# Performance work log

Measured on AMD Instinct MI355X. Metric: run time of the kernel, lower is better.

The kernel has to match this reference:

```python
import jax, jax.numpy as jnp
import numpy as np

N_GENE, N_CPG, N_MIRNA = 20000, 60000, 2000
HID, H, NL = 128, 8, 2
C = HID // H
B = 64
NEG_SLOPE = 0.2
LN_EPS = 1e-5
# edge types in HeteroConv order: (src_node_idx, dst_node_idx); node order: 0=gene,1=cpg,2=mirna
EDGE_META = [(1, 0), (0, 1), (2, 0), (0, 2), (0, 0), (0, 0), (1, 1), (2, 2)]


def layernorm(x, g, b):
    mu = jnp.mean(x, axis=-1, keepdims=True)
    var = jnp.mean(jnp.square(x - mu), axis=-1, keepdims=True)
    return (x - mu) * jax.lax.rsqrt(var + LN_EPS) * g + b


def gatv2_conv(x_src, x_dst, ei, Wl, Wr, att, bias):
    """PyG GATv2Conv, add_self_loops=False, concat heads, eval mode (no dropout)."""
    src, dst = ei[0], ei[1]
    n_dst = x_dst.shape[0]
    hs = (x_src @ Wl).reshape(-1, H, C)   # lin_l -> source features [Ns,H,C]
    hd = (x_dst @ Wr).reshape(-1, H, C)   # lin_r -> target features [Nd,H,C]
    e = jax.nn.leaky_relu(hs[src] + hd[dst], NEG_SLOPE)   # [E,H,C]
    logits = jnp.einsum('ehc,hc->eh', e, att)             # [E,H]
    # segment softmax over destination nodes
    m = jax.ops.segment_max(logits, dst, num_segments=n_dst)
    a = jnp.exp(logits - m[dst])
    s = jax.ops.segment_sum(a, dst, num_segments=n_dst)
    alpha = a / (s[dst] + 1e-16)                          # [E,H]
    msg = (hs[src] * alpha[:, :, None]).reshape(-1, HID)  # [E,HID]
    out = jax.ops.segment_sum(msg, dst, num_segments=n_dst)
    return out + bias


def setup_inputs() -> dict:
    key = jax.random.key(0)
    ks = list(jax.random.split(key, 40))
    nk = lambda: ks.pop()
    rn = lambda shape, s=0.05: jax.random.normal(nk(), shape, jnp.float32) * s

    def edges(E, Ns, Nd):
        src = jax.random.randint(nk(), (E,), 0, Ns, jnp.int32)
        dst = jax.random.randint(nk(), (E,), 0, Nd, jnp.int32)
        return jnp.stack([src, dst])

    def self_loops(N):
        ar = jnp.arange(N, dtype=jnp.int32)
        return jnp.stack([ar, ar])

    inp = {
        'batch_gene': rn((B, N_GENE), 1.0),
        'batch_meth': rn((B, N_CPG), 1.0),
        'batch_mirna': rn((B, N_MIRNA), 1.0),
        'emb_gene': rn((N_GENE, HID)),
        'emb_cpg': rn((N_CPG, HID)),
        'emb_mirna': rn((N_MIRNA, HID)),
        'Wl': rn((NL, 8, HID, HID)),
        'Wr': rn((NL, 8, HID, HID)),
        'att': rn((NL, 8, H, C)),
        'bias': rn((NL, 8, HID), 0.01),
        'ln_gamma': jnp.ones((NL, 3, HID), jnp.float32),
        'ln_beta': jnp.zeros((NL, 3, HID), jnp.float32),
        'out_gamma': jnp.ones((3, HID), jnp.float32),
        'out_beta': jnp.zeros((3, HID), jnp.float32),
        'ei_cg': edges(500000, N_CPG, N_GENE),
        'ei_gc': edges(500000, N_GENE, N_CPG),
        'ei_mg': edges(150000, N_MIRNA, N_GENE),
        'ei_gm': edges(150000, N_GENE, N_MIRNA),
        'ei_gg': edges(500000, N_GENE, N_GENE),
        'ei_sg': self_loops(N_GENE),
        'ei_sc': self_loops(N_CPG),
        'ei_sm': self_loops(N_MIRNA),
    }
    return inp


def forward(batch_gene, batch_meth, batch_mirna, emb_gene, emb_cpg, emb_mirna,
            Wl, Wr, att, bias, ln_gamma, ln_beta, out_gamma, out_beta, edge_list):
    x = [emb_gene, emb_cpg, emb_mirna]  # 0=gene,1=cpg,2=mirna
    for l in range(NL):
        agg = [jnp.zeros_like(x[0]), jnp.zeros_like(x[1]), jnp.zeros_like(x[2])]
        for t, (ei, (si, di)) in enumerate(zip(edge_list, EDGE_META)):
            agg[di] = agg[di] + gatv2_conv(x[si], x[di], ei,
                                           Wl[l, t], Wr[l, t], att[l, t], bias[l, t])
        # ELU + residual + LayerNorm per node type (dropout=0 / eval)
        x = [layernorm(x[i] + jax.nn.elu(agg[i]), ln_gamma[l, i], ln_beta[l, i])
             for i in range(3)]
    z_gene = layernorm(batch_gene @ x[0] / np.sqrt(N_GENE), out_gamma[0], out_beta[0])
    z_cpg = layernorm(batch_meth @ x[1] / np.sqrt(N_CPG), out_gamma[1], out_beta[1])
    z_mirna = layernorm(batch_mirna @ x[2] / np.sqrt(N_MIRNA), out_gamma[2], out_beta[2])
    return (z_gene, z_cpg, z_mirna)


def reference(batch_gene, batch_meth, batch_mirna, emb_gene, emb_cpg, emb_mirna,
              Wl, Wr, att, bias, ln_gamma, ln_beta, out_gamma, out_beta,
              ei_cg, ei_gc, ei_mg, ei_gm, ei_gg, ei_sg, ei_sc, ei_sm):
    edge_list = [ei_cg, ei_gc, ei_mg, ei_gm, ei_gg, ei_sg, ei_sc, ei_sm]
    return forward(batch_gene, batch_meth, batch_mirna, emb_gene, emb_cpg, emb_mirna,
                   Wl, Wr, att, bias, ln_gamma, ln_beta, out_gamma, out_beta, edge_list)
```

## Files before the change

kernel.cpp:

```cpp
#include <hip/hip_runtime.h>
#include <math.h>

typedef __attribute__((ext_vector_type(4))) float f32x4;
typedef __attribute__((ext_vector_type(2))) float f32x2;
typedef __attribute__((ext_vector_type(8))) short bf16x8;

__device__ __forceinline__ float b2f(unsigned short u) {
  return __uint_as_float(((unsigned)u) << 16);
}
__device__ __forceinline__ unsigned short f2b(float f) {
  unsigned x = __float_as_uint(f);
  unsigned r = (x + 0x7FFFu + ((x >> 16) & 1u)) >> 16;
  return (unsigned short)r;
}
__device__ __forceinline__ f32x2 bf2x2(unsigned u) {
  f32x2 r;
  r.x = __uint_as_float(u << 16);
  r.y = __uint_as_float(u & 0xFFFF0000u);
  return r;
}
__device__ __forceinline__ f32x2 pk_max(f32x2 a, f32x2 b) {
#if __has_builtin(__builtin_elementwise_max)
  return __builtin_elementwise_max(a, b);
#else
  f32x2 r; r.x = fmaxf(a.x, b.x); r.y = fmaxf(a.y, b.y); return r;
#endif
}
__device__ __forceinline__ f32x2 pk_fma(f32x2 a, f32x2 b, f32x2 c) {
#if __has_builtin(__builtin_elementwise_fma)
  return __builtin_elementwise_fma(a, b, c);
#else
  f32x2 r; r.x = fmaf(a.x, b.x, c.x); r.y = fmaf(a.y, b.y, c.y); return r;
#endif
}

#if __has_builtin(__builtin_amdgcn_cvt_pk_f32_fp8)
template<bool HI>
__device__ __forceinline__ f32x2 fp8x2_dec(unsigned w) {
  return __builtin_amdgcn_cvt_pk_f32_fp8(w, HI);
}
#else
__device__ __forceinline__ float fp8_dec1(unsigned b) {
  unsigned s = b >> 7, e = (b >> 3) & 15, m = b & 7;
  float v = (e == 0) ? (float)m * 0.001953125f
                     : __uint_as_float(((e - 7 + 127) << 23) | (m << 20));
  return s ? -v : v;
}
template<bool HI>
__device__ __forceinline__ f32x2 fp8x2_dec(unsigned w) {
  unsigned h = HI ? (w >> 16) : w;
  f32x2 r; r.x = fp8_dec1(h & 0xFF); r.y = fp8_dec1((h >> 8) & 0xFF);
  return r;
}
#endif
#if __has_builtin(__builtin_amdgcn_cvt_pk_fp8_f32)
__device__ __forceinline__ unsigned char fp8_enc_byte(float a) {
  return (unsigned char)(__builtin_amdgcn_cvt_pk_fp8_f32(a, a, 0, false) & 0xFF);
}
#else
__device__ __forceinline__ unsigned fp8_enc1(float f) {
  unsigned s = (__float_as_uint(f) >> 31) << 7;
  float a = fabsf(f);
  if (a >= 448.f) return s | 0x7E;
  if (a < 0.015625f) {
    int m = (int)(a * 512.f + 0.5f);
    return s | (unsigned)(m > 7 ? 7 : m);
  }
  int ex; (void)frexpf(a, &ex);
  int E = ex - 1;
  float sig = a * exp2f((float)(-E));
  int m = (int)((sig - 1.f) * 8.f + 0.5f);
  if (m == 8) { m = 0; E += 1; }
  if (E > 8) return s | 0x7E;
  return s | (unsigned)((E + 7) << 3) | (unsigned)m;
}
__device__ __forceinline__ unsigned char fp8_enc_byte(float a) {
  return (unsigned char)fp8_enc1(a);
}
#endif

__global__ __launch_bounds__(256) void prep_w(
    const float* __restrict__ Wl, const float* __restrict__ Wr,
    unsigned short* __restrict__ wt)
{
  int elem = blockIdx.x * 256 + threadIdx.x;
  int mat = elem >> 14;
  int c = (elem >> 7) & 127;
  int k = elem & 127;
  const float* srcb = (mat & 1) ? Wr : Wl;
  wt[elem] = f2b(srcb[((long)(mat >> 1) << 14) + (k << 7) + c]);
}

__global__ __launch_bounds__(256) void cast_all(
    const float* __restrict__ e0, const float* __restrict__ e1,
    const float* __restrict__ e2, unsigned short* __restrict__ x0,
    unsigned short* __restrict__ x1, unsigned short* __restrict__ x2,
    int n0, int n1, int n2)
{
  int i = blockIdx.x * 256 + threadIdx.x;
  const float* s; unsigned short* d; int loc = i;
  if (loc < n0) { s = e0; d = x0; }
  else {
    loc -= n0;
    if (loc < n1) { s = e1; d = x1; }
    else { loc -= n1; if (loc >= n2) return; s = e2; d = x2; }
  }
  float4 v = *(const float4*)(s + (long)loc * 4);
  ushort4 o = {f2b(v.x), f2b(v.y), f2b(v.z), f2b(v.w)};
  *(ushort4*)(d + (long)loc * 4) = o;
}

__global__ __launch_bounds__(128) void prep_bias(
    const float* __restrict__ bias, float* __restrict__ bsum)
{
  int c = threadIdx.x;
  const int TM[3] = {0x35, 0x42, 0x88};
  for (int l = 0; l < 2; ++l)
    for (int ty = 0; ty < 3; ++ty) {
      float s = 0.f;
      for (int t = 0; t < 8; ++t)
        if (TM[ty] & (1 << t)) s += bias[(l * 8 + t) * 128 + c];
      bsum[(l * 3 + ty) * 128 + c] = s;
    }
}

__device__ __forceinline__ void mproj_tile(
    char* lx, char* lw, const unsigned short* __restrict__ xb,
    const unsigned short* __restrict__ wt, void* __restrict__ outv,
    int N, long r0, int tid, int mode)
{
#pragma unroll
  for (int i = 0; i < 8; ++i) {
    int ch = i * 256 + tid;
    int row = ch >> 4, k0 = (ch & 15) << 3;
    uint4 xv = {0u, 0u, 0u, 0u};
    if (r0 + row < N) xv = *(const uint4*)(xb + (r0 + row) * 128 + k0);
    *(uint4*)(lx + ((row * 256 + k0 * 2) ^ ((row & 7) << 4))) = xv;
    uint4 wv = *(const uint4*)(wt + (long)ch * 8);
    *(uint4*)(lw + ((ch * 16) ^ ((row & 7) << 4))) = wv;
  }
  __syncthreads();

  const int lane = tid & 63;
  const int lr = lane & 15, lk = lane >> 4;
  const int rbase = (tid >> 6) * 32;
  f32x4 acc[2][8] = {};
#pragma unroll
  for (int kb = 0; kb < 4; ++kb) {
    int k = kb * 32 + lk * 8;
    int ra = rbase + lr;
    bf16x8 a0 = *(const bf16x8*)(lx + ((ra * 256 + k * 2) ^ ((ra & 7) << 4)));
    int rb = rbase + 16 + lr;
    bf16x8 a1 = *(const bf16x8*)(lx + ((rb * 256 + k * 2) ^ ((rb & 7) << 4)));
#pragma unroll
    for (int cc = 0; cc < 8; ++cc) {
      int col = cc * 16 + lr;
      bf16x8 bfr = *(const bf16x8*)(lw + ((col * 256 + k * 2) ^ ((col & 7) << 4)));
      acc[0][cc] = __builtin_amdgcn_mfma_f32_16x16x32_bf16(a0, bfr, acc[0][cc], 0, 0, 0);
      acc[1][cc] = __builtin_amdgcn_mfma_f32_16x16x32_bf16(a1, bfr, acc[1][cc], 0, 0, 0);
    }
  }
  __syncthreads();
#pragma unroll
  for (int rt = 0; rt < 2; ++rt) {
    int rowb = rbase + rt * 16 + lk * 4;
#pragma unroll
    for (int cc = 0; cc < 8; ++cc) {
      int col = cc * 16 + lr;
#pragma unroll
      for (int q = 0; q < 4; ++q) {
        long row = r0 + rowb + q;
        if (row < N) {
          if (mode == 3)
            ((unsigned char*)outv)[row * 128 + col] = fp8_enc_byte(acc[rt][cc][q]);
          else if (mode == 2)
            ((unsigned short*)outv)[row * 128 + col] = f2b(acc[rt][cc][q]);
          else
            ((float*)outv)[row * 128 + col] = acc[rt][cc][q];
        }
      }
    }
  }
}

struct PJob { const unsigned short* x; const unsigned short* wt; void* out; int N; int mode; };
struct PArgs { PJob j[13]; int off[14]; };

__global__ __launch_bounds__(256) void mproj_all(PArgs a)
{
  __shared__ __align__(16) char lx[32768];
  __shared__ __align__(16) char lw[32768];
  int blk = blockIdx.x, t = 0;
  while (blk >= a.off[t + 1]) ++t;
  const PJob& J = a.j[t];
  mproj_tile(lx, lw, J.x, J.wt, J.out, J.N, (long)(blk - a.off[t]) * 128,
             threadIdx.x, J.mode);
}

struct BArgs {
  const int* src[5]; const int* dst[5];
  int* cnt[5];
  int* tmp[5];
  int* rs[5];
  int* csrc[5];
  int E[5], Nd[5], NB[5], B[5];
  int cOff[6], fOff[6];
};

__global__ __launch_bounds__(256) void bucket_count(BArgs a)
{
  __shared__ int h[512];
  int blk = blockIdx.x, t = 0;
  while (blk >= a.cOff[t + 1]) ++t;
  int lb = blk - a.cOff[t];
  int B = a.B[t], NB = a.NB[t], E = a.E[t];
  for (int i = threadIdx.x; i < B; i += 256) h[i] = 0;
  __syncthreads();
  const int* dst = a.dst[t];
  int base = lb * 4096;
#pragma unroll
  for (int j = 0; j < 16; ++j) {
    int e = base + j * 256 + threadIdx.x;
    if (e < E) atomicAdd(&h[dst[e] >> 7], 1);
  }
  __syncthreads();
  int* cnt = a.cnt[t];
  for (int b = threadIdx.x; b < B; b += 256) cnt[b * NB + lb] = h[b];
}

__global__ __launch_bounds__(1024) void bucket_scan(BArgs a)
{
  int t = blockIdx.x;
  int n = a.B[t] * a.NB[t];
  int* dp = a.cnt[t];
  __shared__ int wsum[16];
  __shared__ int sbase, ctot;
  int tid = threadIdx.x;
  int lane = tid & 63, wid = tid >> 6;
  if (tid == 0) sbase = 0;
  __syncthreads();
  for (int chunk = 0; chunk < n; chunk += 16384) {
    int idx0 = chunk + tid * 16;
    int v[16], lsum = 0;
#pragma unroll
    for (int j = 0; j < 16; ++j) {
      v[j] = (idx0 + j < n) ? dp[idx0 + j] : 0;
      lsum += v[j];
    }
    int sc = lsum;
#pragma unroll
    for (int o = 1; o < 64; o <<= 1) {
      int u = __shfl_up(sc, o);
      if (lane >= o) sc += u;
    }
    if (lane == 63) wsum[wid] = sc;
    __syncthreads();
    if (wid == 0) {
      int w = (lane < 16) ? wsum[lane] : 0;
      int s2 = w;
#pragma unroll
      for (int o = 1; o < 16; o <<= 1) {
        int u = __shfl_up(s2, o);
        if (lane >= o) s2 += u;
      }
      if (lane < 16) wsum[lane] = s2 - w;
      if (lane == 15) ctot = s2;
    }
    __syncthreads();
    int excl = sbase + wsum[wid] + (sc - lsum);
#pragma unroll
    for (int j = 0; j < 16; ++j) {
      if (idx0 + j < n) dp[idx0 + j] = excl;
      excl += v[j];
    }
    __syncthreads();
    if (tid == 0) sbase += ctot;
    __syncthreads();
  }
}

__global__ __launch_bounds__(256) void bucket_scatter(BArgs a)
{
  __shared__ int cur[512];
  int blk = blockIdx.x, t = 0;
  while (blk >= a.cOff[t + 1]) ++t;
  int lb = blk - a.cOff[t];
  int B = a.B[t], NB = a.NB[t], E = a.E[t];
  const int* cnt = a.cnt[t];
  for (int b = threadIdx.x; b < B; b += 256) cur[b] = cnt[b * NB + lb];
  __syncthreads();
  const int* src = a.src[t];
  const int* dst = a.dst[t];
  int* tmp = a.tmp[t];
  int base = lb * 4096;
#pragma unroll
  for (int j = 0; j < 16; ++j) {
    int e = base + j * 256 + threadIdx.x;
    if (e < E) {
      int dv = dst[e];
      int pos = atomicAdd(&cur[dv >> 7], 1);
      tmp[pos] = ((dv & 127) << 16) | src[e];
    }
  }
}

__global__ __launch_bounds__(256) void bucket_finalize(BArgs a)
{
  __shared__ int h[128], sc[128], ex[128], cur[128];
  int blk = blockIdx.x, t = 0;
  while (blk >= a.fOff[t + 1]) ++t;
  int b = blk - a.fOff[t];
  int B = a.B[t], NB = a.NB[t], E = a.E[t], Nd = a.Nd[t];
  const int* cnt = a.cnt[t];
  const int* tmp = a.tmp[t];
  int* rs = a.rs[t];
  int* csrc = a.csrc[t];
  int tid = threadIdx.x;
  int beg = cnt[b * NB];
  int end = (b + 1 < B) ? cnt[(b + 1) * NB] : E;
  if (tid < 128) h[tid] = 0;
  __syncthreads();
  for (int i = beg + tid; i < end; i += 256)
    atomicAdd(&h[tmp[i] >> 16], 1);
  __syncthreads();
  if (tid < 128) sc[tid] = h[tid];
  __syncthreads();
#pragma unroll
  for (int off = 1; off < 128; off <<= 1) {
    int v = (tid < 128 && tid >= off) ? sc[tid - off] : 0;
    __syncthreads();
    if (tid < 128) sc[tid] += v;
    __syncthreads();
  }
  if (tid < 128) {
    ex[tid] = sc[tid] - h[tid];
    cur[tid] = 0;
    int dg = b * 128 + tid;
    if (dg < Nd) rs[dg] = beg + ex[tid];
  }
  if (b == B - 1 && tid == 0) rs[Nd] = E;
  __syncthreads();
  for (int i = beg + tid; i < end; i += 256) {
    int v = tmp[i];
    int d = v >> 16;
    int r = atomicAdd(&cur[d], 1);
    csrc[beg + ex[d] + r] = v & 0xFFFF;
  }
}

struct GSeg {
  const int* rs[3]; const int* csrc[3];
  const unsigned char* hs[3]; const unsigned short* hd[3];
  const float* att[3];
  const float* aggSelf;
  const float* xin;
  float* xf; unsigned short* xb;
  const float* bsum;
  const float* gam; const float* bet;
  int Nd; int ntypes;
};
struct GArgs { GSeg s[3]; int off[4]; };

__global__ __launch_bounds__(256) void gat_gather_ln(GArgs g)
{
  int blk = blockIdx.x, si = 0;
  while (blk >= g.off[si + 1]) ++si;
  const GSeg& sg = g.s[si];
  int d = (blk - g.off[si]) * 4 + (threadIdx.x >> 6);
  if (d >= sg.Nd) return;
  int lane = threadIdx.x & 63;
  int q = lane >> 4, j = lane & 15;
  f32x2 T0 = {0.f, 0.f}, T1 = {0.f, 0.f}, T2 = {0.f, 0.f}, T3 = {0.f, 0.f};
  for (int k = 0; k < sg.ntypes; ++k) {
    const float* ap = sg.att[k] + 8 * j;
    float4 aa = *(const float4*)ap;
    float4 ab = *(const float4*)(ap + 4);
    f32x2 A0 = {aa.x, aa.y}, A1 = {aa.z, aa.w};
    f32x2 A2 = {ab.x, ab.y}, A3 = {ab.z, ab.w};
    uint4 hu = *((const uint4*)(sg.hd[k] + (long)d * 128) + j);
    f32x2 H0 = bf2x2(hu.x), H1 = bf2x2(hu.y);
    f32x2 H2 = bf2x2(hu.z), H3 = bf2x2(hu.w);
    const int* cs = sg.csrc[k];
    const unsigned char* hsk = sg.hs[k];
    int beg = sg.rs[k][d], end = sg.rs[k][d + 1];
    f32x2 n0 = {0.f, 0.f}, n1 = {0.f, 0.f}, n2 = {0.f, 0.f}, n3 = {0.f, 0.f};
    float D = 0.f;

#define GA_EDGE(U)                                                          \
    {                                                                       \
      f32x2 h0 = fp8x2_dec<false>((U).x), h1 = fp8x2_dec<true>((U).x);      \
      f32x2 h2 = fp8x2_dec<false>((U).y), h3 = fp8x2_dec<true>((U).y);      \
      f32x2 v0 = h0 + H0, v1 = h1 + H1, v2 = h2 + H2, v3 = h3 + H3;         \
      v0 = pk_max(v0, v0 * 0.2f);                                           \
      v1 = pk_max(v1, v1 * 0.2f);                                           \
      v2 = pk_max(v2, v2 * 0.2f);                                           \
      v3 = pk_max(v3, v3 * 0.2f);                                           \
      f32x2 pv = pk_fma(v0, A0, pk_fma(v1, A1, pk_fma(v2, A2, v3 * A3)));   \
      float p = pv.x + pv.y;                                                \
      p += __shfl_xor(p, 1);                                                \
      float a = __expf(fminf(p, 60.f));                                     \
      f32x2 av = {a, a};                                                    \
      n0 = pk_fma(h0, av, n0);                                              \
      n1 = pk_fma(h1, av, n1);                                              \
      n2 = pk_fma(h2, av, n2);                                              \
      n3 = pk_fma(h3, av, n3);                                              \
      D += a;                                                               \
    }

    int i = beg + q;
    int sA = (i < end) ? cs[i] : 0;
    int sB = (i + 4 < end) ? cs[i + 4] : 0;
    for (; i + 4 < end; i += 8) {
      uint2 u0 = *((const uint2*)(hsk + (long)sA * 128) + j);
      uint2 u1 = *((const uint2*)(hsk + (long)sB * 128) + j);
      sA = (i + 8 < end) ? cs[i + 8] : 0;
      sB = (i + 12 < end) ? cs[i + 12] : 0;
      GA_EDGE(u0);
      GA_EDGE(u1);
    }
    if (i < end) {
      uint2 u = *((const uint2*)(hsk + (long)sA * 128) + j);
      GA_EDGE(u);
    }
#undef GA_EDGE

#pragma unroll
    for (int o = 16; o < 64; o <<= 1) {
      n0.x += __shfl_xor(n0.x, o); n0.y += __shfl_xor(n0.y, o);
      n1.x += __shfl_xor(n1.x, o); n1.y += __shfl_xor(n1.y, o);
      n2.x += __shfl_xor(n2.x, o); n2.y += __shfl_xor(n2.y, o);
      n3.x += __shfl_xor(n3.x, o); n3.y += __shfl_xor(n3.y, o);
      D += __shfl_xor(D, o);
    }
    float inv = 1.f / (D + 1e-16f);
    f32x2 iv = {inv, inv};
    T0 = pk_fma(n0, iv, T0);
    T1 = pk_fma(n1, iv, T1);
    T2 = pk_fma(n2, iv, T2);
    T3 = pk_fma(n3, iv, T3);
  }

  long base = (long)d * 128 + 8 * j;
  float4 sA0 = *(const float4*)(sg.aggSelf + base);
  float4 sA1 = *(const float4*)(sg.aggSelf + base + 4);
  float4 bb0 = *(const float4*)(sg.bsum + 8 * j);
  float4 bb1 = *(const float4*)(sg.bsum + 8 * j + 4);
  float v[8];
  v[0] = sA0.x + T0.x + bb0.x; v[1] = sA0.y + T0.y + bb0.y;
  v[2] = sA0.z + T1.x + bb0.z; v[3] = sA0.w + T1.y + bb0.w;
  v[4] = sA1.x + T2.x + bb1.x; v[5] = sA1.y + T2.y + bb1.y;
  v[6] = sA1.z + T3.x + bb1.z; v[7] = sA1.w + T3.y + bb1.w;
#pragma unroll
  for (int c = 0; c < 8; ++c) v[c] = v[c] > 0.f ? v[c] : __expf(v[c]) - 1.f;
  float4 xi0 = *(const float4*)(sg.xin + base);
  float4 xi1 = *(const float4*)(sg.xin + base + 4);
  float xr[8] = {xi0.x + v[0], xi0.y + v[1], xi0.z + v[2], xi0.w + v[3],
                 xi1.x + v[4], xi1.y + v[5], xi1.z + v[6], xi1.w + v[7]};
  float ssum = ((xr[0] + xr[1]) + (xr[2] + xr[3])) +
               ((xr[4] + xr[5]) + (xr[6] + xr[7]));
#pragma unroll
  for (int o = 1; o < 16; o <<= 1) ssum += __shfl_xor(ssum, o);
  float mu = ssum * 0.0078125f;
  float qs = 0.f;
#pragma unroll
  for (int c = 0; c < 8; ++c) { float dd = xr[c] - mu; qs += dd * dd; }
#pragma unroll
  for (int o = 1; o < 16; o <<= 1) qs += __shfl_xor(qs, o);
  float rr = rsqrtf(qs * 0.0078125f + 1e-5f);
  float4 g0 = *(const float4*)(sg.gam + 8 * j);
  float4 g1 = *(const float4*)(sg.gam + 8 * j + 4);
  float4 e0 = *(const float4*)(sg.bet + 8 * j);
  float4 e1 = *(const float4*)(sg.bet + 8 * j + 4);
  float y[8];
  y[0] = (xr[0] - mu) * rr * g0.x + e0.x;
  y[1] = (xr[1] - mu) * rr * g0.y + e0.y;
  y[2] = (xr[2] - mu) * rr * g0.z + e0.z;
  y[3] = (xr[3] - mu) * rr * g0.w + e0.w;
  y[4] = (xr[4] - mu) * rr * g1.x + e1.x;
  y[5] = (xr[5] - mu) * rr * g1.y + e1.y;
  y[6] = (xr[6] - mu) * rr * g1.z + e1.z;
  y[7] = (xr[7] - mu) * rr * g1.w + e1.w;
  if (q == 0) {
    float4 o0 = {y[0], y[1], y[2], y[3]};
    float4 o1 = {y[4], y[5], y[6], y[7]};
    *(float4*)(sg.xf + base) = o0;
    *(float4*)(sg.xf + base + 4) = o1;
    uint4 ub;
    ub.x = (unsigned)f2b(y[0]) | ((unsigned)f2b(y[1]) << 16);
    ub.y = (unsigned)f2b(y[2]) | ((unsigned)f2b(y[3]) << 16);
    ub.z = (unsigned)f2b(y[4]) | ((unsigned)f2b(y[5]) << 16);
    ub.w = (unsigned)f2b(y[6]) | ((unsigned)f2b(y[7]) << 16);
    *(uint4*)(sg.xb + base) = ub;
  }
}

struct ZArgs {
  const float* batch[3]; const float* x[3]; float* zp[3]; int N[3];
  int off[4];
};

__global__ __launch_bounds__(256) void zgemm_all(ZArgs z)
{
  __shared__ __align__(16) float xl[64 * 128];
  __shared__ __align__(16) float bl[64 * 65];
  int blk = blockIdx.x, s = 0;
  while (blk >= z.off[s + 1]) ++s;
  int chunk = blk - z.off[s];
  const float* batch = z.batch[s];
  const float* x = z.x[s];
  int N = z.N[s];
  int tid = threadIdx.x;
  int n0 = chunk * 64;
  for (int i = tid; i < 64 * 128; i += 256) {
    int nn = i >> 7;
    xl[i] = (n0 + nn < N) ? x[(long)(n0 + nn) * 128 + (i & 127)] : 0.f;
  }
  for (int i = tid; i < 64 * 64; i += 256) {
    int b = i >> 6, nn = i & 63;
    bl[nn * 65 + b] = (n0 + nn < N) ? batch[(long)b * N + n0 + nn] : 0.f;
  }
  __syncthreads();
  int cg = (tid & 31) * 4;
  int bg = (tid >> 5) * 8;
  float acc[8][4] = {};
  for (int nn = 0; nn < 64; ++nn) {
    float4 xv = *(const float4*)(xl + nn * 128 + cg);
#pragma unroll
    for (int i = 0; i < 8; ++i) {
      float bv = bl[nn * 65 + bg + i];
      acc[i][0] = fmaf(bv, xv.x, acc[i][0]);
      acc[i][1] = fmaf(bv, xv.y, acc[i][1]);
      acc[i][2] = fmaf(bv, xv.z, acc[i][2]);
      acc[i][3] = fmaf(bv, xv.w, acc[i][3]);
    }
  }
  float* zp = z.zp[s] + (long)chunk * 8192;
#pragma unroll
  for (int i = 0; i < 8; ++i) {
    float4 v = {acc[i][0], acc[i][1], acc[i][2], acc[i][3]};
    *(float4*)(zp + (bg + i) * 128 + cg) = v;
  }
}

__global__ __launch_bounds__(256) void zfinal(
    const float* __restrict__ zp0, const float* __restrict__ zp1,
    const float* __restrict__ zp2, int G0, int G1, int G2,
    float s0, float s1, float s2, const float* __restrict__ gam,
    const float* __restrict__ bet, float* __restrict__ out)
{
  int blk = blockIdx.x;
  int ty = blk >> 4;
  int rowL = (blk & 15) * 4 + (threadIdx.x >> 6);
  int lane = threadIdx.x & 63;
  const float* zp = ty == 0 ? zp0 : (ty == 1 ? zp1 : zp2);
  int G = ty == 0 ? G0 : (ty == 1 ? G1 : G2);
  float sc = ty == 0 ? s0 : (ty == 1 ? s1 : s2);
  long i0 = rowL * 128 + lane, i1 = i0 + 64;
  float a0[8], a1[8];
#pragma unroll
  for (int u = 0; u < 8; ++u) { a0[u] = 0.f; a1[u] = 0.f; }
  int g = 0;
  for (; g + 8 <= G; g += 8) {
#pragma unroll
    for (int u = 0; u < 8; ++u) {
      a0[u] += zp[(long)(g + u) * 8192 + i0];
      a1[u] += zp[(long)(g + u) * 8192 + i1];
    }
  }
  for (; g < G; ++g) { a0[0] += zp[(long)g * 8192 + i0]; a1[0] += zp[(long)g * 8192 + i1]; }
  float x0 = (((a0[0] + a0[1]) + (a0[2] + a0[3])) + ((a0[4] + a0[5]) + (a0[6] + a0[7]))) * sc;
  float x1 = (((a1[0] + a1[1]) + (a1[2] + a1[3])) + ((a1[4] + a1[5]) + (a1[6] + a1[7]))) * sc;
  float s = x0 + x1;
#pragma unroll
  for (int o = 32; o > 0; o >>= 1) s += __shfl_xor(s, o);
  float mu = s * 0.0078125f;
  float d0 = x0 - mu, d1 = x1 - mu;
  float qv = d0 * d0 + d1 * d1;
#pragma unroll
  for (int o = 32; o > 0; o >>= 1) qv += __shfl_xor(qv, o);
  float r = rsqrtf(qv * 0.0078125f + 1e-5f);
  long base = (long)(ty * 64 + rowL) * 128;
  out[base + lane]      = d0 * r * gam[ty * 128 + lane]      + bet[ty * 128 + lane];
  out[base + 64 + lane] = d1 * r * gam[ty * 128 + 64 + lane] + bet[ty * 128 + 64 + lane];
}

extern "C" void kernel_launch(void* const* d_in, const int* in_sizes, int n_in,
                              void* d_out, int out_size, void* d_ws, size_t ws_size,
                              hipStream_t stream)
{
  const float* batchp[3] = {(const float*)d_in[0], (const float*)d_in[1],
                            (const float*)d_in[2]};
  const float* emb[3] = {(const float*)d_in[3], (const float*)d_in[4],
                         (const float*)d_in[5]};
  const float* Wl   = (const float*)d_in[6];
  const float* Wr   = (const float*)d_in[7];
  const float* att  = (const float*)d_in[8];
  const float* bias = (const float*)d_in[9];
  const float* lng  = (const float*)d_in[10];
  const float* lnb  = (const float*)d_in[11];
  const float* outg = (const float*)d_in[12];
  const float* outb = (const float*)d_in[13];
  const int* eiP[8]; int E[8];
  for (int t = 0; t < 8; ++t) { eiP[t] = (const int*)d_in[14 + t]; E[t] = in_sizes[14 + t] / 2; }
  int Nn[3] = {in_sizes[3] / 128, in_sizes[4] / 128, in_sizes[5] / 128};
  long Ntot = (long)Nn[0] + Nn[1] + Nn[2];

  const int SI[5] = {1, 0, 2, 0, 0};
  const int DI[5] = {0, 1, 0, 2, 0};

  char* p = (char*)d_ws;
  auto carve = [&](size_t b) -> void* {
    void* r = (void*)p; p += (b + 255) & ~(size_t)255; return r;
  };
  float* xf[3];
  for (int ty = 0; ty < 3; ++ty) xf[ty] = (float*)carve((size_t)Nn[ty] * 128 * 4);
  unsigned short* xb[3];
  for (int ty = 0; ty < 3; ++ty) xb[ty] = (unsigned short*)carve((size_t)Nn[ty] * 128 * 2);
  float* aggAll = (float*)carve((size_t)Ntot * 128 * 4);
  float* agg[3] = {aggAll, aggAll + (long)Nn[0] * 128, aggAll + ((long)Nn[0] + Nn[1]) * 128};
  unsigned short* hdT[5];
  char* projRegion = p;
  for (int t = 0; t < 5; ++t) hdT[t] = (unsigned short*)carve((size_t)Nn[DI[t]] * 128 * 2);
  long hsElems = 0;
  for (int t = 0; t < 5; ++t) hsElems += (long)Nn[SI[t]] * 128;
  unsigned char* hs8base = (unsigned char*)carve((size_t)hsElems);
  unsigned char* hs8T[5];
  {
    unsigned char* q8 = hs8base;
    for (int t = 0; t < 5; ++t) { hs8T[t] = q8; q8 += (long)Nn[SI[t]] * 128; }
  }
  float* bsumBuf = (float*)carve(2 * 3 * 128 * 4);
  unsigned short* wtb = (unsigned short*)carve((size_t)32 * 16384 * 2);

  int nch[3];
  for (int ty = 0; ty < 3; ++ty) nch[ty] = (Nn[ty] + 63) / 64;
  float* zpBase = (float*)carve((size_t)(nch[0] + nch[1] + nch[2]) * 8192 * 4);
  float* zp[3];
  zp[0] = zpBase;
  zp[1] = zp[0] + (long)nch[0] * 8192;
  zp[2] = zp[1] + (long)nch[1] * 8192;
  (void)projRegion;

  BArgs ba;
  {
    int cOff = 0, fOff = 0;
    for (int t = 0; t < 5; ++t) {
      int nd = Nn[DI[t]];
      ba.src[t] = eiP[t];
      ba.dst[t] = eiP[t] + E[t];
      ba.E[t] = E[t];
      ba.Nd[t] = nd;
      ba.NB[t] = (E[t] + 4095) / 4096;
      ba.B[t] = (nd + 127) / 128;
      ba.cnt[t] = (int*)carve((size_t)ba.B[t] * ba.NB[t] * 4);
      ba.tmp[t] = (int*)carve((size_t)E[t] * 4);
      ba.rs[t] = (int*)carve((size_t)(nd + 1) * 4);
      ba.csrc[t] = (int*)carve((size_t)E[t] * 4);
      ba.cOff[t] = cOff; cOff += ba.NB[t];
      ba.fOff[t] = fOff; fOff += ba.B[t];
    }
    ba.cOff[5] = cOff;
    ba.fOff[5] = fOff;
  }
  if ((size_t)(p - (char*)d_ws) > ws_size) return;

  auto WTB = [&](int l, int t, int which) {
    return wtb + ((long)((l * 8 + t) * 2 + which) << 14);
  };

  prep_w<<<2048, 256, 0, stream>>>(Wl, Wr, wtb);
  {
    int n0 = Nn[0] * 32, n1 = Nn[1] * 32, n2 = Nn[2] * 32;
    cast_all<<<(int)((n0 + n1 + n2 + 255) / 256), 256, 0, stream>>>(
        emb[0], emb[1], emb[2], xb[0], xb[1], xb[2], n0, n1, n2);
  }
  prep_bias<<<1, 128, 0, stream>>>(bias, bsumBuf);

  bucket_count<<<ba.cOff[5], 256, 0, stream>>>(ba);
  bucket_scan<<<5, 1024, 0, stream>>>(ba);
  bucket_scatter<<<ba.cOff[5], 256, 0, stream>>>(ba);
  bucket_finalize<<<ba.fOff[5], 256, 0, stream>>>(ba);

  const int GT[3][3] = {{0, 2, 4}, {1, -1, -1}, {3, -1, -1}};
  const int GN[3] = {3, 1, 1};

  for (int l = 0; l < 2; ++l) {
    const float* xinf[3] = {l == 0 ? emb[0] : xf[0],
                            l == 0 ? emb[1] : xf[1],
                            l == 0 ? emb[2] : xf[2]};
    PArgs pa;
    {
      int off = 0, j = 0;
      auto add = [&](const unsigned short* x, const unsigned short* wt,
                     void* out, int N, int mode) {
        pa.j[j] = {x, wt, out, N, mode};
        pa.off[j] = off;
        off += (N + 127) / 128;
        ++j;
      };
      for (int t = 0; t < 5; ++t) add(xb[SI[t]], WTB(l, t, 0), hs8T[t], Nn[SI[t]], 3);
      for (int t = 0; t < 5; ++t) add(xb[DI[t]], WTB(l, t, 1), hdT[t], Nn[DI[t]], 2);
      for (int ty = 0; ty < 3; ++ty) add(xb[ty], WTB(l, 5 + ty, 0), agg[ty], Nn[ty], 0);
      pa.off[13] = off;
      mproj_all<<<off, 256, 0, stream>>>(pa);
    }
    GArgs ga;
    {
      int off = 0;
      for (int s = 0; s < 3; ++s) {
        GSeg& sg = ga.s[s];
        sg.aggSelf = agg[s];
        sg.xin = xinf[s];
        sg.xf = xf[s];
        sg.xb = xb[s];
        sg.bsum = bsumBuf + (long)(l * 3 + s) * 128;
        sg.gam = lng + (long)(l * 3 + s) * 128;
        sg.bet = lnb + (long)(l * 3 + s) * 128;
        sg.Nd = Nn[s];
        sg.ntypes = GN[s];
        for (int k = 0; k < GN[s]; ++k) {
          int t = GT[s][k];
          sg.rs[k] = ba.rs[t];
          sg.csrc[k] = ba.csrc[t];
          sg.hs[k] = hs8T[t];
          sg.hd[k] = hdT[t];
          sg.att[k] = att + (long)(l * 8 + t) * 128;
        }
        ga.off[s] = off;
        off += (Nn[s] + 3) / 4;
      }
      ga.off[3] = off;
      gat_gather_ln<<<off, 256, 0, stream>>>(ga);
    }
  }

  ZArgs za;
  {
    int off = 0;
    for (int ty = 0; ty < 3; ++ty) {
      za.batch[ty] = batchp[ty];
      za.x[ty] = xf[ty];
      za.zp[ty] = zp[ty];
      za.N[ty] = Nn[ty];
      za.off[ty] = off;
      off += nch[ty];
    }
    za.off[3] = off;
    zgemm_all<<<off, 256, 0, stream>>>(za);
  }
  zfinal<<<48, 256, 0, stream>>>(
      zp[0], zp[1], zp[2], nch[0], nch[1], nch[2],
      (float)(1.0 / sqrt((double)Nn[0])), (float)(1.0 / sqrt((double)Nn[1])),
      (float)(1.0 / sqrt((double)Nn[2])), outg, outb, (float*)d_out);
}
```

Measured before the change: 560.3 us.

## Reuse staged input tile across multiple weight projections per block

The projection kernel now loads each 128-row bf16 input tile into shared memory once and loops over up to four weight matrices that share that input, writing each output in its own format. Before, every projection re-read the same input rows from global memory in a separate block. This cuts redundant input reads. In exchange there are fewer, longer blocks (gene rows split into two jobs of 4 and 3 weights), which lowers parallelism and adds extra barriers between weight reloads.

```diff
diff --git a/kernel.cpp b/kernel.cpp
--- a/kernel.cpp
+++ b/kernel.cpp
@@ -124,77 +124,87 @@
     }
 }
 
-__device__ __forceinline__ void mproj_tile(
-    char* lx, char* lw, const unsigned short* __restrict__ xb,
-    const unsigned short* __restrict__ wt, void* __restrict__ outv,
-    int N, long r0, int tid, int mode)
-{
+struct MPJob {
+  const unsigned short* x; int N; int nw;
+  const unsigned short* wt[4]; void* out[4]; int mode[4];
+};
+struct MPArgs { MPJob j[4]; int off[5]; };
+
+__global__ __launch_bounds__(256) void mproj_multi(MPArgs a)
+{
+  __shared__ __align__(16) char lx[32768];
+  __shared__ __align__(16) char lw[32768];
+  int blk = blockIdx.x, t = 0;
+  while (blk >= a.off[t + 1]) ++t;
+  const MPJob& J = a.j[t];
+  const long r0 = (long)(blk - a.off[t]) * 128;
+  const int tid = threadIdx.x;
+  const int N = J.N;
+
 #pragma unroll
   for (int i = 0; i < 8; ++i) {
     int ch = i * 256 + tid;
     int row = ch >> 4, k0 = (ch & 15) << 3;
     uint4 xv = {0u, 0u, 0u, 0u};
-    if (r0 + row < N) xv = *(const uint4*)(xb + (r0 + row) * 128 + k0);
+    if (r0 + row < N) xv = *(const uint4*)(J.x + (r0 + row) * 128 + k0);
     *(uint4*)(lx + ((row * 256 + k0 * 2) ^ ((row & 7) << 4))) = xv;
-    uint4 wv = *(const uint4*)(wt + (long)ch * 8);
-    *(uint4*)(lw + ((ch * 16) ^ ((row & 7) << 4))) = wv;
-  }
-  __syncthreads();
+  }
 
   const int lane = tid & 63;
   const int lr = lane & 15, lk = lane >> 4;
   const int rbase = (tid >> 6) * 32;
-  f32x4 acc[2][8] = {};
-#pragma unroll
-  for (int kb = 0; kb < 4; ++kb) {
-    int k = kb * 32 + lk * 8;
-    int ra = rbase + lr;
-    bf16x8 a0 = *(const bf16x8*)(lx + ((ra * 256 + k * 2) ^ ((ra & 7) << 4)));
-    int rb = rbase + 16 + lr;
-    bf16x8 a1 = *(const bf16x8*)(lx + ((rb * 256 + k * 2) ^ ((rb & 7) << 4)));
-#pragma unroll
-    for (int cc = 0; cc < 8; ++cc) {
-      int col = cc * 16 + lr;
-      bf16x8 bfr = *(const bf16x8*)(lw + ((col * 256 + k * 2) ^ ((col & 7) << 4)));
-      acc[0][cc] = __builtin_amdgcn_mfma_f32_16x16x32_bf16(a0, bfr, acc[0][cc], 0, 0, 0);
-      acc[1][cc] = __builtin_amdgcn_mfma_f32_16x16x32_bf16(a1, bfr, acc[1][cc], 0, 0, 0);
-    }
-  }
-  __syncthreads();
-#pragma unroll
-  for (int rt = 0; rt < 2; ++rt) {
-    int rowb = rbase + rt * 16 + lk * 4;
-#pragma unroll
-    for (int cc = 0; cc < 8; ++cc) {
-      int col = cc * 16 + lr;
-#pragma unroll
-      for (int q = 0; q < 4; ++q) {
-        long row = r0 + rowb + q;
-        if (row < N) {
-          if (mode == 3)
-            ((unsigned char*)outv)[row * 128 + col] = fp8_enc_byte(acc[rt][cc][q]);
-          else if (mode == 2)
-            ((unsigned short*)outv)[row * 128 + col] = f2b(acc[rt][cc][q]);
-          else
-            ((float*)outv)[row * 128 + col] = acc[rt][cc][q];
+
+  for (int w = 0; w < J.nw; ++w) {
+    __syncthreads();
+    const unsigned short* wt = J.wt[w];
+#pragma unroll
+    for (int i = 0; i < 8; ++i) {
+      int ch = i * 256 + tid;
+      int row = ch >> 4;
+      uint4 wv = *(const uint4*)(wt + (long)ch * 8);
+      *(uint4*)(lw + ((ch * 16) ^ ((row & 7) << 4))) = wv;
+    }
+    __syncthreads();
+
+    f32x4 acc[2][8] = {};
+#pragma unroll
+    for (int kb = 0; kb < 4; ++kb) {
+      int k = kb * 32 + lk * 8;
+      int ra = rbase + lr;
+      bf16x8 a0 = *(const bf16x8*)(lx + ((ra * 256 + k * 2) ^ ((ra & 7) << 4)));
+      int rb = rbase + 16 + lr;
+      bf16x8 a1 = *(const bf16x8*)(lx + ((rb * 256 + k * 2) ^ ((rb & 7) << 4)));
+#pragma unroll
+      for (int cc = 0; cc < 8; ++cc) {
+        int col = cc * 16 + lr;
+        bf16x8 bfr = *(const bf16x8*)(lw + ((col * 256 + k * 2) ^ ((col & 7) << 4)));
+        acc[0][cc] = __builtin_amdgcn_mfma_f32_16x16x32_bf16(a0, bfr, acc[0][cc], 0, 0, 0);
+        acc[1][cc] = __builtin_amdgcn_mfma_f32_16x16x32_bf16(a1, bfr, acc[1][cc], 0, 0, 0);
+      }
+    }
+    int mode = J.mode[w];
+    void* outv = J.out[w];
+#pragma unroll
+    for (int rt = 0; rt < 2; ++rt) {
+      int rowb = rbase + rt * 16 + lk * 4;
+#pragma unroll
+      for (int cc = 0; cc < 8; ++cc) {
+        int col = cc * 16 + lr;
+#pragma unroll
+        for (int q = 0; q < 4; ++q) {
+          long row = r0 + rowb + q;
+          if (row < N) {
+            if (mode == 3)
+              ((unsigned char*)outv)[row * 128 + col] = fp8_enc_byte(acc[rt][cc][q]);
+            else if (mode == 2)
+              ((unsigned short*)outv)[row * 128 + col] = f2b(acc[rt][cc][q]);
+            else
+              ((float*)outv)[row * 128 + col] = acc[rt][cc][q];
+          }
         }
       }
     }
   }
-}
-
-struct PJob { const unsigned short* x; const unsigned short* wt; void* out; int N; int mode; };
-struct PArgs { PJob j[13]; int off[14]; };
-
-__global__ __launch_bounds__(256) void mproj_all(PArgs a)
-{
-  __shared__ __align__(16) char lx[32768];
-  __shared__ __align__(16) char lw[32768];
-  int blk = blockIdx.x, t = 0;
-  while (blk >= a.off[t + 1]) ++t;
-  const PJob& J = a.j[t];
-  mproj_tile(lx, lw, J.x, J.wt, J.out, J.N, (long)(blk - a.off[t]) * 128,
-             threadIdx.x, J.mode);
 }
 
 struct BArgs {
@@ -619,7 +629,6 @@
   float* aggAll = (float*)carve((size_t)Ntot * 128 * 4);
   float* agg[3] = {aggAll, aggAll + (long)Nn[0] * 128, aggAll + ((long)Nn[0] + Nn[1]) * 128};
   unsigned short* hdT[5];
-  char* projRegion = p;
   for (int t = 0; t < 5; ++t) hdT[t] = (unsigned short*)carve((size_t)Nn[DI[t]] * 128 * 2);
   long hsElems = 0;
   for (int t = 0; t < 5; ++t) hsElems += (long)Nn[SI[t]] * 128;
@@ -639,7 +648,6 @@
   zp[0] = zpBase;
   zp[1] = zp[0] + (long)nch[0] * 8192;
   zp[2] = zp[1] + (long)nch[1] * 8192;
-  (void)projRegion;
 
   BArgs ba;
   {
@@ -688,21 +696,37 @@
     const float* xinf[3] = {l == 0 ? emb[0] : xf[0],
                             l == 0 ? emb[1] : xf[1],
                             l == 0 ? emb[2] : xf[2]};
-    PArgs pa;
+    MPArgs mp;
     {
-      int off = 0, j = 0;
-      auto add = [&](const unsigned short* x, const unsigned short* wt,
-                     void* out, int N, int mode) {
-        pa.j[j] = {x, wt, out, N, mode};
-        pa.off[j] = off;
-        off += (N + 127) / 128;
-        ++j;
+      int off = 0, nj = 0;
+      auto addJob = [&](const unsigned short* x, int N) {
+        mp.j[nj].x = x; mp.j[nj].N = N; mp.j[nj].nw = 0;
+        mp.off[nj] = off; off += (N + 127) / 128;
+        return nj++;
       };
-      for (int t = 0; t < 5; ++t) add(xb[SI[t]], WTB(l, t, 0), hs8T[t], Nn[SI[t]], 3);
-      for (int t = 0; t < 5; ++t) add(xb[DI[t]], WTB(l, t, 1), hdT[t], Nn[DI[t]], 2);
-      for (int ty = 0; ty < 3; ++ty) add(xb[ty], WTB(l, 5 + ty, 0), agg[ty], Nn[ty], 0);
-      pa.off[13] = off;
-      mproj_all<<<off, 256, 0, stream>>>(pa);
+      auto addW = [&](int ji, const unsigned short* wt, void* out, int mode) {
+        MPJob& J = mp.j[ji];
+        J.wt[J.nw] = wt; J.out[J.nw] = out; J.mode[J.nw] = mode; J.nw++;
+      };
+      int ga_ = addJob(xb[0], Nn[0]);
+      addW(ga_, WTB(l, 1, 0), hs8T[1], 3);
+      addW(ga_, WTB(l, 3, 0), hs8T[3], 3);
+      addW(ga_, WTB(l, 4, 0), hs8T[4], 3);
+      addW(ga_, WTB(l, 0, 1), hdT[0], 2);
+      int gb_ = addJob(xb[0], Nn[0]);
+      addW(gb_, WTB(l, 2, 1), hdT[2], 2);
+      addW(gb_, WTB(l, 4, 1), hdT[4], 2);
+      addW(gb_, WTB(l, 5, 0), agg[0], 0);
+      int cj_ = addJob(xb[1], Nn[1]);
+      addW(cj_, WTB(l, 0, 0), hs8T[0], 3);
+      addW(cj_, WTB(l, 1, 1), hdT[1], 2);
+      addW(cj_, WTB(l, 6, 0), agg[1], 0);
+      int mj_ = addJob(xb[2], Nn[2]);
+      addW(mj_, WTB(l, 2, 0), hs8T[2], 3);
+      addW(mj_, WTB(l, 3, 1), hdT[3], 2);
+      addW(mj_, WTB(l, 7, 0), agg[2], 0);
+      mp.off[4] = off;
+      mproj_multi<<<off, 256, 0, stream>>>(mp);
     }
     GArgs ga;
     {
```

Result: no change. 554.3 us (-1.1%).
